# Optimization experiments

Measured on AMD Instinct MI355X. Metric: run time of the kernel, lower is better.

The kernel has to match this reference:

```python
import jax, jax.numpy as jnp
import numpy as np

N_NODES = 100000
N_EDGES = 1600000
IN_DIM, HID_DIM, OUT_DIM = 64, 64, 32


def setup_inputs() -> dict:
    key = jax.random.key(0)
    ks = jax.random.split(key, 8)
    s_in = 1.0 / np.sqrt(IN_DIM)
    s_hid = 1.0 / np.sqrt(HID_DIM)
    return {
        "x": jax.random.normal(ks[0], (N_NODES, IN_DIM), dtype=jnp.float32),
        "edge_index": jax.random.randint(ks[1], (2, N_EDGES), 0, N_NODES, dtype=jnp.int64),
        "W1l": jax.random.uniform(ks[2], (IN_DIM, HID_DIM), jnp.float32, -s_in, s_in),
        "b1l": jnp.zeros((HID_DIM,), jnp.float32),
        "W1r": jax.random.uniform(ks[3], (IN_DIM, HID_DIM), jnp.float32, -s_in, s_in),
        "W2l": jax.random.uniform(ks[4], (HID_DIM, OUT_DIM), jnp.float32, -s_hid, s_hid),
        "b2l": jnp.zeros((OUT_DIM,), jnp.float32),
        "W2r": jax.random.uniform(ks[5], (HID_DIM, OUT_DIM), jnp.float32, -s_hid, s_hid),
    }


def sage_conv(x, src, dst, W_l, b_l, W_r, n_nodes):
    # PyG SAGEConv (aggr='mean'): lin_l(mean of neighbor msgs) + lin_r(x)
    msg = x[src]                                                    # [E, d] gather
    agg = jax.ops.segment_sum(msg, dst, num_segments=n_nodes)      # [N, d] scatter-add
    deg = jax.ops.segment_sum(jnp.ones_like(dst, dtype=x.dtype), dst,
                              num_segments=n_nodes)
    agg = agg / jnp.maximum(deg, 1.0)[:, None]                     # mean (0 for isolated)
    return agg @ W_l + b_l + x @ W_r


def reference(x, edge_index, W1l, b1l, W1r, W2l, b2l, W2r):
    src, dst = edge_index[0], edge_index[1]
    n = x.shape[0]
    h = jax.nn.relu(sage_conv(x, src, dst, W1l, b1l, W1r, n))
    return sage_conv(h, src, dst, W2l, b2l, W2r, n)
```

## Files before the change

### kernel.cpp

```cpp
#include <hip/hip_runtime.h>

#define N_NODES 100000
#define N_EDGES 1600000
#define B2_SHIFT 9
#define BUCK_N (1 << B2_SHIFT)
#define NB2 ((N_NODES + BUCK_N - 1) >> B2_SHIFT)
#define BCAP 9216
#define PAIR_EPB 4096
#define PAIR_BLOCKS ((N_EDGES + PAIR_EPB - 1) / PAIR_EPB)
#define CAST_BLOCKS 6250
#define PREP_BLOCKS (PAIR_BLOCKS + 1 + CAST_BLOCKS)

typedef __attribute__((ext_vector_type(8))) short bf16x8;
typedef __attribute__((ext_vector_type(4))) float f32x4;

__device__ __forceinline__ unsigned pack2(float a, float b) {
    unsigned ua = __float_as_uint(a), ub = __float_as_uint(b);
    ua = (ua + 0x7FFFu + ((ua >> 16) & 1u)) >> 16;
    ub = (ub + 0x7FFFu + ((ub >> 16) & 1u)) >> 16;
    return ua | (ub << 16);
}
__device__ __forceinline__ float lo16(unsigned u) { return __uint_as_float(u << 16); }
__device__ __forceinline__ float hi16(unsigned u) { return __uint_as_float(u & 0xFFFF0000u); }

__global__ __launch_bounds__(256) void k_prep(
    const float* __restrict__ x, const int* __restrict__ ei,
    const float* __restrict__ W1l, const float* __restrict__ W1r,
    const float* __restrict__ W2l, const float* __restrict__ W2r,
    unsigned* __restrict__ xh, int* __restrict__ bcur,
    int* __restrict__ pairs, uint4* __restrict__ wf)
{
    __shared__ int lh[2][NB2];
    __shared__ int lb[2][NB2];

    if (blockIdx.x < PAIR_BLOCKS) {
        for (int i = threadIdx.x; i < NB2; i += 256) { lh[0][i] = 0; lh[1][i] = 0; }
        __syncthreads();
        int cp = (threadIdx.x >> 6) & 1;
        int base = blockIdx.x * PAIR_EPB;
        int myb[16], myr[16], myp[16];
#pragma unroll
        for (int t = 0; t < 16; t++) {
            int e = base + t * 256 + threadIdx.x;
            myb[t] = -1;
            if (e < N_EDGES) {
                int dst = ei[N_EDGES + e];
                int b = dst >> B2_SHIFT;
                myb[t] = b;
                myr[t] = atomicAdd(&lh[cp][b], 1);
                myp[t] = (ei[e] << B2_SHIFT) | (dst & (BUCK_N - 1));
            }
        }
        __syncthreads();
        for (int i = threadIdx.x; i < NB2; i += 256) {
            int c0 = lh[0][i], c1 = lh[1][i];
            int basei = (c0 + c1) ? atomicAdd(&bcur[i], c0 + c1) : 0;
            lb[0][i] = basei;
            lb[1][i] = basei + c0;
        }
        __syncthreads();
#pragma unroll
        for (int t = 0; t < 16; t++) {
            if (myb[t] >= 0) {
                int slot = lb[cp][myb[t]] + myr[t];
                if (slot < BCAP)
                    pairs[myb[t] * BCAP + slot] = myp[t];
            }
        }
    } else if (blockIdx.x == PAIR_BLOCKS) {
        for (int s = threadIdx.x; s < 1536; s += 256) {
            int f = s >> 6, l = s & 63;
            int m = l & 15, q = l >> 4;
            float w[8];
            if (f < 16) {
                int jt = f >> 2, ks = f & 3;
                int j = jt * 16 + m;
                int k0 = ks * 32 + q * 8;
#pragma unroll
                for (int i = 0; i < 8; i++) {
                    int kk = k0 + i;
                    w[i] = (kk < 64) ? W1l[kk * 64 + j] : W1r[(kk - 64) * 64 + j];
                }
            } else {
                int f2 = f - 16;
                int jt = f2 >> 1, ks = f2 & 1;
                int j = jt * 16 + m;
                int k0 = ks * 32 + q * 8;
#pragma unroll
                for (int i = 0; i < 8; i++) {
                    int kk = k0 + i;
                    w[i] = (j < 32) ? W2l[kk * 32 + j] : W2r[kk * 32 + (j - 32)];
                }
            }
            wf[s] = make_uint4(pack2(w[0], w[1]), pack2(w[2], w[3]),
                               pack2(w[4], w[5]), pack2(w[6], w[7]));
        }
    } else {
        int i = (blockIdx.x - PAIR_BLOCKS - 1) * 256 + threadIdx.x;
        if (i < N_NODES * 16) {
            float4 v = ((const float4*)x)[i];
            ((uint2*)xh)[i] = make_uint2(pack2(v.x, v.y), pack2(v.z, v.w));
        }
    }
}

__global__ __launch_bounds__(512) void k_sortb(const int* __restrict__ bcur,
                                               const int* __restrict__ pairs,
                                               int* __restrict__ sorted_src,
                                               int* __restrict__ rs,
                                               int* __restrict__ re)
{
    __shared__ int sp[BCAP];
    __shared__ int lcnt[BUCK_N];
    __shared__ int wtot[8];
    int b = blockIdx.x;
    int beg = b * BCAP;
    int cnt = bcur[b];
    if (cnt > BCAP) cnt = BCAP;
    for (int i = threadIdx.x; i < cnt; i += 512) sp[i] = pairs[beg + i];
    lcnt[threadIdx.x] = 0;
    __syncthreads();
    for (int i = threadIdx.x; i < cnt; i += 512)
        atomicAdd(&lcnt[sp[i] & (BUCK_N - 1)], 1);
    __syncthreads();
    int v = lcnt[threadIdx.x];
    int lane = threadIdx.x & 63, wid = threadIdx.x >> 6;
    int s = v;
#pragma unroll
    for (int off = 1; off < 64; off <<= 1) {
        int t = __shfl_up(s, off);
        if (lane >= off) s += t;
    }
    if (lane == 63) wtot[wid] = s;
    __syncthreads();
    int woff = 0;
#pragma unroll
    for (int k = 0; k < 8; k++) woff += (k < wid) ? wtot[k] : 0;
    int excl = woff + s - v;
    int n = (b << B2_SHIFT) + threadIdx.x;
    if (n < N_NODES) { rs[n] = beg + excl; re[n] = beg + excl + v; }
    __syncthreads();
    lcnt[threadIdx.x] = beg + excl;
    __syncthreads();
    for (int i = threadIdx.x; i < cnt; i += 512) {
        int p = sp[i];
        int idx = atomicAdd(&lcnt[p & (BUCK_N - 1)], 1);
        sorted_src[idx] = p >> B2_SHIFT;
    }
}

__global__ __launch_bounds__(256) void k_agg1(const int* __restrict__ rs,
                                              const int* __restrict__ re,
                                              const int* __restrict__ sorted_src,
                                              const unsigned* __restrict__ xh,
                                              unsigned* __restrict__ agg1h)
{
    int node = blockIdx.x * 8 + (threadIdx.x >> 5);
    if (node >= N_NODES) return;
    int d2 = threadIdx.x & 31;
    int beg = rs[node], end = re[node];
    float a0 = 0.f, a1 = 0.f, b0 = 0.f, b1 = 0.f;
    int idx = beg;
    for (; idx + 8 <= end; idx += 8) {
        int s0 = sorted_src[idx + 0], s1 = sorted_src[idx + 1];
        int s2 = sorted_src[idx + 2], s3 = sorted_src[idx + 3];
        int s4 = sorted_src[idx + 4], s5 = sorted_src[idx + 5];
        int s6 = sorted_src[idx + 6], s7 = sorted_src[idx + 7];
        unsigned p0 = xh[(size_t)s0 * 32 + d2];
        unsigned p1 = xh[(size_t)s1 * 32 + d2];
        unsigned p2 = xh[(size_t)s2 * 32 + d2];
        unsigned p3 = xh[(size_t)s3 * 32 + d2];
        unsigned p4 = xh[(size_t)s4 * 32 + d2];
        unsigned p5 = xh[(size_t)s5 * 32 + d2];
        unsigned p6 = xh[(size_t)s6 * 32 + d2];
        unsigned p7 = xh[(size_t)s7 * 32 + d2];
        a0 += lo16(p0) + lo16(p1);  a1 += hi16(p0) + hi16(p1);
        b0 += lo16(p2) + lo16(p3);  b1 += hi16(p2) + hi16(p3);
        a0 += lo16(p4) + lo16(p5);  a1 += hi16(p4) + hi16(p5);
        b0 += lo16(p6) + lo16(p7);  b1 += hi16(p6) + hi16(p7);
    }
    for (; idx + 2 <= end; idx += 2) {
        int s0 = sorted_src[idx], s1 = sorted_src[idx + 1];
        unsigned p0 = xh[(size_t)s0 * 32 + d2];
        unsigned p1 = xh[(size_t)s1 * 32 + d2];
        a0 += lo16(p0) + lo16(p1);  a1 += hi16(p0) + hi16(p1);
    }
    if (idx < end) {
        unsigned p = xh[(size_t)sorted_src[idx] * 32 + d2];
        a0 += lo16(p);  a1 += hi16(p);
    }
    agg1h[(size_t)node * 32 + d2] = pack2(a0 + b0, a1 + b1);
}

#define TPW 2
#define NTILE ((N_NODES + 15) / 16)
#define NODE_BLOCKS (((NTILE + TPW - 1) / TPW + 3) / 4)
__global__ __launch_bounds__(256) void k_node_mfma(
    const unsigned* __restrict__ xh, const unsigned* __restrict__ agg1h,
    const int* __restrict__ rs, const int* __restrict__ re,
    const float* __restrict__ b1l, const uint4* __restrict__ wf,
    unsigned* __restrict__ t2h, float* __restrict__ t3)
{
    __shared__ uint4 sWF[24 * 64];
    __shared__ float sH[4][16 * 68];
    __shared__ float sT[4][16 * 44];

    for (int s = threadIdx.x; s < 1536; s += 256)
        sWF[s] = wf[s];
    __syncthreads();

    int w = threadIdx.x >> 6, lane = threadIdx.x & 63;
    int m = lane & 15, q = lane >> 4;

    bf16x8 WF1[4][4], WF2[4][2];
#pragma unroll
    for (int jt = 0; jt < 4; jt++) {
#pragma unroll
        for (int ks = 0; ks < 4; ks++)
            WF1[jt][ks] = __builtin_bit_cast(bf16x8, sWF[(jt * 4 + ks) * 64 + lane]);
#pragma unroll
        for (int ks = 0; ks < 2; ks++)
            WF2[jt][ks] = __builtin_bit_cast(bf16x8, sWF[(16 + jt * 2 + ks) * 64 + lane]);
    }
    float bias[4];
#pragma unroll
    for (int jt = 0; jt < 4; jt++) bias[jt] = b1l[jt * 16 + m];

    float* myH = &sH[w][0];
    float* myT = &sT[w][0];
    int gw = blockIdx.x * 4 + w;

    for (int t = 0; t < TPW; t++) {
        int tile = gw * TPW + t;
        if (tile >= NTILE) break;
        int nb = tile * 16;

        int nc = nb + m; if (nc >= N_NODES) nc = N_NODES - 1;
        const uint4* arow = (const uint4*)(agg1h + (size_t)nc * 32);
        const uint4* xrow = (const uint4*)(xh + (size_t)nc * 32);
        bf16x8 AM[2], AX[2];
        AM[0] = __builtin_bit_cast(bf16x8, arow[q]);
        AM[1] = __builtin_bit_cast(bf16x8, arow[4 + q]);
        AX[0] = __builtin_bit_cast(bf16x8, xrow[q]);
        AX[1] = __builtin_bit_cast(bf16x8, xrow[4 + q]);

        float invr[4];
#pragma unroll
        for (int r = 0; r < 4; r++) {
            int nn = nb + q * 4 + r;
            int nc2 = (nn < N_NODES) ? nn : 0;
            invr[r] = 1.0f / fmaxf((float)(re[nc2] - rs[nc2]), 1.0f);
        }

#pragma unroll
        for (int jt = 0; jt < 4; jt++) {
            f32x4 aM = {0.f, 0.f, 0.f, 0.f}, aX = {0.f, 0.f, 0.f, 0.f};
            aM = __builtin_amdgcn_mfma_f32_16x16x32_bf16(AM[0], WF1[jt][0], aM, 0, 0, 0);
            aM = __builtin_amdgcn_mfma_f32_16x16x32_bf16(AM[1], WF1[jt][1], aM, 0, 0, 0);
            aX = __builtin_amdgcn_mfma_f32_16x16x32_bf16(AX[0], WF1[jt][2], aX, 0, 0, 0);
            aX = __builtin_amdgcn_mfma_f32_16x16x32_bf16(AX[1], WF1[jt][3], aX, 0, 0, 0);
#pragma unroll
            for (int r = 0; r < 4; r++) {
                float hv = fmaxf(aM[r] * invr[r] + aX[r] + bias[jt], 0.0f);
                myH[(q * 4 + r) * 68 + jt * 16 + m] = hv;
            }
        }

        bf16x8 A2[2];
#pragma unroll
        for (int ks = 0; ks < 2; ks++) {
            const float* p = &myH[m * 68 + ks * 32 + q * 8];
            float4 v0 = *(const float4*)p;
            float4 v1 = *(const float4*)(p + 4);
            uint4 u = make_uint4(pack2(v0.x, v0.y), pack2(v0.z, v0.w),
                                 pack2(v1.x, v1.y), pack2(v1.z, v1.w));
            A2[ks] = __builtin_bit_cast(bf16x8, u);
        }

#pragma unroll
        for (int jt = 0; jt < 4; jt++) {
            f32x4 acc = {0.f, 0.f, 0.f, 0.f};
            acc = __builtin_amdgcn_mfma_f32_16x16x32_bf16(A2[0], WF2[jt][0], acc, 0, 0, 0);
            acc = __builtin_amdgcn_mfma_f32_16x16x32_bf16(A2[1], WF2[jt][1], acc, 0, 0, 0);
            if (jt < 2) {
#pragma unroll
                for (int r = 0; r < 4; r++)
                    myT[(q * 4 + r) * 44 + jt * 16 + m] = acc[r];
            } else {
#pragma unroll
                for (int r = 0; r < 4; r++) {
                    int nn = nb + q * 4 + r;
                    if (nn < N_NODES)
                        t3[(size_t)nn * 32 + (jt - 2) * 16 + m] = acc[r];
                }
            }
        }

        int ni = lane >> 2, u4g = lane & 3;
        const float* tp = &myT[ni * 44 + u4g * 8];
        float4 a = *(const float4*)tp;
        float4 b = *(const float4*)(tp + 4);
        if (nb + ni < N_NODES) {
            uint4 o = make_uint4(pack2(a.x, a.y), pack2(a.z, a.w),
                                 pack2(b.x, b.y), pack2(b.z, b.w));
            *(uint4*)(t2h + (size_t)(nb + ni) * 16 + u4g * 4) = o;
        }
    }
}

__global__ __launch_bounds__(256) void k_agg2out(
    const int* __restrict__ rs, const int* __restrict__ re,
    const int* __restrict__ sorted_src,
    const unsigned* __restrict__ t2h, const float* __restrict__ t3,
    const float* __restrict__ b2l, float* __restrict__ out)
{
    int node = blockIdx.x * 16 + (threadIdx.x >> 4);
    if (node >= N_NODES) return;
    int d2 = threadIdx.x & 15;
    int beg = rs[node], end = re[node];
    float a0 = 0.f, a1 = 0.f, b0 = 0.f, b1 = 0.f;
    int idx = beg;
    for (; idx + 8 <= end; idx += 8) {
        int s0 = sorted_src[idx + 0], s1 = sorted_src[idx + 1];
        int s2 = sorted_src[idx + 2], s3 = sorted_src[idx + 3];
        int s4 = sorted_src[idx + 4], s5 = sorted_src[idx + 5];
        int s6 = sorted_src[idx + 6], s7 = sorted_src[idx + 7];
        unsigned p0 = t2h[(size_t)s0 * 16 + d2];
        unsigned p1 = t2h[(size_t)s1 * 16 + d2];
        unsigned p2 = t2h[(size_t)s2 * 16 + d2];
        unsigned p3 = t2h[(size_t)s3 * 16 + d2];
        unsigned p4 = t2h[(size_t)s4 * 16 + d2];
        unsigned p5 = t2h[(size_t)s5 * 16 + d2];
        unsigned p6 = t2h[(size_t)s6 * 16 + d2];
        unsigned p7 = t2h[(size_t)s7 * 16 + d2];
        a0 += lo16(p0) + lo16(p1);  a1 += hi16(p0) + hi16(p1);
        b0 += lo16(p2) + lo16(p3);  b1 += hi16(p2) + hi16(p3);
        a0 += lo16(p4) + lo16(p5);  a1 += hi16(p4) + hi16(p5);
        b0 += lo16(p6) + lo16(p7);  b1 += hi16(p6) + hi16(p7);
    }
    for (; idx + 2 <= end; idx += 2) {
        int s0 = sorted_src[idx], s1 = sorted_src[idx + 1];
        unsigned p0 = t2h[(size_t)s0 * 16 + d2];
        unsigned p1 = t2h[(size_t)s1 * 16 + d2];
        a0 += lo16(p0) + lo16(p1);  a1 += hi16(p0) + hi16(p1);
    }
    if (idx < end) {
        unsigned p = t2h[(size_t)sorted_src[idx] * 16 + d2];
        a0 += lo16(p);  a1 += hi16(p);
    }
    float inv = 1.0f / fmaxf((float)(end - beg), 1.0f);
    float2 tv = ((const float2*)(t3 + (size_t)node * 32))[d2];
    float2 bv = ((const float2*)b2l)[d2];
    ((float2*)(out + (size_t)node * 32))[d2] =
        make_float2((a0 + b0) * inv + tv.x + bv.x,
                    (a1 + b1) * inv + tv.y + bv.y);
}

extern "C" void kernel_launch(void* const* d_in, const int* in_sizes, int n_in,
                              void* d_out, int out_size, void* d_ws, size_t ws_size,
                              hipStream_t stream) {
    const float* x   = (const float*)d_in[0];
    const int*   ei  = (const int*)d_in[1];
    const float* W1l = (const float*)d_in[2];
    const float* b1l = (const float*)d_in[3];
    const float* W1r = (const float*)d_in[4];
    const float* W2l = (const float*)d_in[5];
    const float* b2l = (const float*)d_in[6];
    const float* W2r = (const float*)d_in[7];
    float* out = (float*)d_out;

    const size_t N = N_NODES;
    int* wsi = (int*)d_ws;
    int*      pairs      = wsi;
    int*      sorted_src = wsi + 1806336;
    int*      bcur       = wsi + 3612672;
    int*      rs         = wsi + 3612928;
    int*      re         = wsi + 3712928;
    unsigned* xh         = (unsigned*)(wsi + 3812928);
    unsigned* t2h        = xh + 32 * N;
    unsigned* agg1h      = t2h + 16 * N;
    float*    t3         = (float*)(agg1h + 32 * N);
    uint4*    wf         = (uint4*)(t3 + 32 * N);

    hipMemsetAsync(bcur, 0, NB2 * sizeof(int), stream);
    k_prep <<<PREP_BLOCKS, 256, 0, stream>>>(x, ei, W1l, W1r, W2l, W2r,
                                             xh, bcur, pairs, wf);
    k_sortb<<<NB2, 512, 0, stream>>>(bcur, pairs, sorted_src, rs, re);

    k_agg1     <<<(int)((N + 7) / 8), 256, 0, stream>>>(rs, re, sorted_src, xh, agg1h);
    k_node_mfma<<<NODE_BLOCKS, 256, 0, stream>>>(xh, agg1h, rs, re,
                                                 b1l, wf, t2h, t3);
    k_agg2out  <<<(int)((N + 15) / 16), 256, 0, stream>>>(rs, re, sorted_src,
                                                 t2h, t3, b2l, out);
}
```

Baseline: 200.2 us.

## Fuse layer-1 neighbor aggregation into the MFMA node kernel

Measured after the change: 259.0 us. 29.4% more time.

```diff
diff --git a/kernel.cpp b/kernel.cpp
--- a/kernel.cpp
+++ b/kernel.cpp
@@ -149,56 +149,15 @@
     }
 }
 
-__global__ __launch_bounds__(256) void k_agg1(const int* __restrict__ rs,
-                                              const int* __restrict__ re,
-                                              const int* __restrict__ sorted_src,
-                                              const unsigned* __restrict__ xh,
-                                              unsigned* __restrict__ agg1h)
-{
-    int node = blockIdx.x * 8 + (threadIdx.x >> 5);
-    if (node >= N_NODES) return;
-    int d2 = threadIdx.x & 31;
-    int beg = rs[node], end = re[node];
-    float a0 = 0.f, a1 = 0.f, b0 = 0.f, b1 = 0.f;
-    int idx = beg;
-    for (; idx + 8 <= end; idx += 8) {
-        int s0 = sorted_src[idx + 0], s1 = sorted_src[idx + 1];
-        int s2 = sorted_src[idx + 2], s3 = sorted_src[idx + 3];
-        int s4 = sorted_src[idx + 4], s5 = sorted_src[idx + 5];
-        int s6 = sorted_src[idx + 6], s7 = sorted_src[idx + 7];
-        unsigned p0 = xh[(size_t)s0 * 32 + d2];
-        unsigned p1 = xh[(size_t)s1 * 32 + d2];
-        unsigned p2 = xh[(size_t)s2 * 32 + d2];
-        unsigned p3 = xh[(size_t)s3 * 32 + d2];
-        unsigned p4 = xh[(size_t)s4 * 32 + d2];
-        unsigned p5 = xh[(size_t)s5 * 32 + d2];
-        unsigned p6 = xh[(size_t)s6 * 32 + d2];
-        unsigned p7 = xh[(size_t)s7 * 32 + d2];
-        a0 += lo16(p0) + lo16(p1);  a1 += hi16(p0) + hi16(p1);
-        b0 += lo16(p2) + lo16(p3);  b1 += hi16(p2) + hi16(p3);
-        a0 += lo16(p4) + lo16(p5);  a1 += hi16(p4) + hi16(p5);
-        b0 += lo16(p6) + lo16(p7);  b1 += hi16(p6) + hi16(p7);
-    }
-    for (; idx + 2 <= end; idx += 2) {
-        int s0 = sorted_src[idx], s1 = sorted_src[idx + 1];
-        unsigned p0 = xh[(size_t)s0 * 32 + d2];
-        unsigned p1 = xh[(size_t)s1 * 32 + d2];
-        a0 += lo16(p0) + lo16(p1);  a1 += hi16(p0) + hi16(p1);
-    }
-    if (idx < end) {
-        unsigned p = xh[(size_t)sorted_src[idx] * 32 + d2];
-        a0 += lo16(p);  a1 += hi16(p);
-    }
-    agg1h[(size_t)node * 32 + d2] = pack2(a0 + b0, a1 + b1);
-}
-
 #define TPW 2
 #define NTILE ((N_NODES + 15) / 16)
 #define NODE_BLOCKS (((NTILE + TPW - 1) / TPW + 3) / 4)
 __global__ __launch_bounds__(256) void k_node_mfma(
-    const unsigned* __restrict__ xh, const unsigned* __restrict__ agg1h,
+    const unsigned* __restrict__ xh,
     const int* __restrict__ rs, const int* __restrict__ re,
-    const float* __restrict__ b1l, const uint4* __restrict__ wf,
+    const int* __restrict__ sorted_src,
+    const float* __restrict__ b1l, const float* __restrict__ b2l,
+    const uint4* __restrict__ wf,
     unsigned* __restrict__ t2h, float* __restrict__ t3)
 {
     __shared__ uint4 sWF[24 * 64];
@@ -211,20 +170,12 @@
 
     int w = threadIdx.x >> 6, lane = threadIdx.x & 63;
     int m = lane & 15, q = lane >> 4;
-
-    bf16x8 WF1[4][4], WF2[4][2];
-#pragma unroll
-    for (int jt = 0; jt < 4; jt++) {
-#pragma unroll
-        for (int ks = 0; ks < 4; ks++)
-            WF1[jt][ks] = __builtin_bit_cast(bf16x8, sWF[(jt * 4 + ks) * 64 + lane]);
-#pragma unroll
-        for (int ks = 0; ks < 2; ks++)
-            WF2[jt][ks] = __builtin_bit_cast(bf16x8, sWF[(16 + jt * 2 + ks) * 64 + lane]);
-    }
+    int half = lane >> 5, d2g = lane & 31;
+
     float bias[4];
 #pragma unroll
     for (int jt = 0; jt < 4; jt++) bias[jt] = b1l[jt * 16 + m];
+    float bias2[2] = { b2l[m], b2l[16 + m] };
 
     float* myH = &sH[w][0];
     float* myT = &sT[w][0];
@@ -235,12 +186,57 @@
         if (tile >= NTILE) break;
         int nb = tile * 16;
 
+        for (int p = 0; p < 8; p++) {
+            int node = nb + 2 * p + half;
+            float a0 = 0.f, a1 = 0.f, c0 = 0.f, c1 = 0.f;
+            if (node < N_NODES) {
+                int beg = rs[node], end = re[node];
+                int idx = beg;
+                for (; idx + 8 <= end; idx += 8) {
+                    int s0 = sorted_src[idx + 0], s1 = sorted_src[idx + 1];
+                    int s2 = sorted_src[idx + 2], s3 = sorted_src[idx + 3];
+                    int s4 = sorted_src[idx + 4], s5 = sorted_src[idx + 5];
+                    int s6 = sorted_src[idx + 6], s7 = sorted_src[idx + 7];
+                    unsigned p0 = xh[(size_t)s0 * 32 + d2g];
+                    unsigned p1 = xh[(size_t)s1 * 32 + d2g];
+                    unsigned p2 = xh[(size_t)s2 * 32 + d2g];
+                    unsigned p3 = xh[(size_t)s3 * 32 + d2g];
+                    unsigned p4 = xh[(size_t)s4 * 32 + d2g];
+                    unsigned p5 = xh[(size_t)s5 * 32 + d2g];
+                    unsigned p6 = xh[(size_t)s6 * 32 + d2g];
+                    unsigned p7 = xh[(size_t)s7 * 32 + d2g];
+                    a0 += lo16(p0) + lo16(p1);  a1 += hi16(p0) + hi16(p1);
+                    c0 += lo16(p2) + lo16(p3);  c1 += hi16(p2) + hi16(p3);
+                    a0 += lo16(p4) + lo16(p5);  a1 += hi16(p4) + hi16(p5);
+                    c0 += lo16(p6) + lo16(p7);  c1 += hi16(p6) + hi16(p7);
+                }
+                for (; idx + 2 <= end; idx += 2) {
+                    int s0 = sorted_src[idx], s1 = sorted_src[idx + 1];
+                    unsigned p0 = xh[(size_t)s0 * 32 + d2g];
+                    unsigned p1 = xh[(size_t)s1 * 32 + d2g];
+                    a0 += lo16(p0) + lo16(p1);  a1 += hi16(p0) + hi16(p1);
+                }
+                if (idx < end) {
+                    unsigned p0 = xh[(size_t)sorted_src[idx] * 32 + d2g];
+                    a0 += lo16(p0);  a1 += hi16(p0);
+                }
+            }
+            *(float2*)&myH[(2 * p + half) * 68 + 2 * d2g] =
+                make_float2(a0 + c0, a1 + c1);
+        }
+
         int nc = nb + m; if (nc >= N_NODES) nc = N_NODES - 1;
-        const uint4* arow = (const uint4*)(agg1h + (size_t)nc * 32);
+        bf16x8 AM[2], AX[2];
+#pragma unroll
+        for (int ks = 0; ks < 2; ks++) {
+            const float* pH = &myH[m * 68 + ks * 32 + q * 8];
+            float4 v0 = *(const float4*)pH;
+            float4 v1 = *(const float4*)(pH + 4);
+            uint4 u = make_uint4(pack2(v0.x, v0.y), pack2(v0.z, v0.w),
+                                 pack2(v1.x, v1.y), pack2(v1.z, v1.w));
+            AM[ks] = __builtin_bit_cast(bf16x8, u);
+        }
         const uint4* xrow = (const uint4*)(xh + (size_t)nc * 32);
-        bf16x8 AM[2], AX[2];
-        AM[0] = __builtin_bit_cast(bf16x8, arow[q]);
-        AM[1] = __builtin_bit_cast(bf16x8, arow[4 + q]);
         AX[0] = __builtin_bit_cast(bf16x8, xrow[q]);
         AX[1] = __builtin_bit_cast(bf16x8, xrow[4 + q]);
 
@@ -255,10 +251,14 @@
 #pragma unroll
         for (int jt = 0; jt < 4; jt++) {
             f32x4 aM = {0.f, 0.f, 0.f, 0.f}, aX = {0.f, 0.f, 0.f, 0.f};
-            aM = __builtin_amdgcn_mfma_f32_16x16x32_bf16(AM[0], WF1[jt][0], aM, 0, 0, 0);
-            aM = __builtin_amdgcn_mfma_f32_16x16x32_bf16(AM[1], WF1[jt][1], aM, 0, 0, 0);
-            aX = __builtin_amdgcn_mfma_f32_16x16x32_bf16(AX[0], WF1[jt][2], aX, 0, 0, 0);
-            aX = __builtin_amdgcn_mfma_f32_16x16x32_bf16(AX[1], WF1[jt][3], aX, 0, 0, 0);
+            aM = __builtin_amdgcn_mfma_f32_16x16x32_bf16(
+                AM[0], __builtin_bit_cast(bf16x8, sWF[(jt * 4 + 0) * 64 + lane]), aM, 0, 0, 0);
+            aM = __builtin_amdgcn_mfma_f32_16x16x32_bf16(
+                AM[1], __builtin_bit_cast(bf16x8, sWF[(jt * 4 + 1) * 64 + lane]), aM, 0, 0, 0);
+            aX = __builtin_amdgcn_mfma_f32_16x16x32_bf16(
+                AX[0], __builtin_bit_cast(bf16x8, sWF[(jt * 4 + 2) * 64 + lane]), aX, 0, 0, 0);
+            aX = __builtin_amdgcn_mfma_f32_16x16x32_bf16(
+                AX[1], __builtin_bit_cast(bf16x8, sWF[(jt * 4 + 3) * 64 + lane]), aX, 0, 0, 0);
 #pragma unroll
             for (int r = 0; r < 4; r++) {
                 float hv = fmaxf(aM[r] * invr[r] + aX[r] + bias[jt], 0.0f);
@@ -280,8 +280,10 @@
 #pragma unroll
         for (int jt = 0; jt < 4; jt++) {
             f32x4 acc = {0.f, 0.f, 0.f, 0.f};
-            acc = __builtin_amdgcn_mfma_f32_16x16x32_bf16(A2[0], WF2[jt][0], acc, 0, 0, 0);
-            acc = __builtin_amdgcn_mfma_f32_16x16x32_bf16(A2[1], WF2[jt][1], acc, 0, 0, 0);
+            acc = __builtin_amdgcn_mfma_f32_16x16x32_bf16(
+                A2[0], __builtin_bit_cast(bf16x8, sWF[(16 + jt * 2 + 0) * 64 + lane]), acc, 0, 0, 0);
+            acc = __builtin_amdgcn_mfma_f32_16x16x32_bf16(
+                A2[1], __builtin_bit_cast(bf16x8, sWF[(16 + jt * 2 + 1) * 64 + lane]), acc, 0, 0, 0);
             if (jt < 2) {
 #pragma unroll
                 for (int r = 0; r < 4; r++)
@@ -291,7 +293,7 @@
                 for (int r = 0; r < 4; r++) {
                     int nn = nb + q * 4 + r;
                     if (nn < N_NODES)
-                        t3[(size_t)nn * 32 + (jt - 2) * 16 + m] = acc[r];
+                        t3[(size_t)nn * 32 + (jt - 2) * 16 + m] = acc[r] + bias2[jt - 2];
                 }
             }
         }
@@ -312,7 +314,7 @@
     const int* __restrict__ rs, const int* __restrict__ re,
     const int* __restrict__ sorted_src,
     const unsigned* __restrict__ t2h, const float* __restrict__ t3,
-    const float* __restrict__ b2l, float* __restrict__ out)
+    float* __restrict__ out)
 {
     int node = blockIdx.x * 16 + (threadIdx.x >> 4);
     if (node >= N_NODES) return;
@@ -350,10 +352,9 @@
     }
     float inv = 1.0f / fmaxf((float)(end - beg), 1.0f);
     float2 tv = ((const float2*)(t3 + (size_t)node * 32))[d2];
-    float2 bv = ((const float2*)b2l)[d2];
     ((float2*)(out + (size_t)node * 32))[d2] =
-        make_float2((a0 + b0) * inv + tv.x + bv.x,
-                    (a1 + b1) * inv + tv.y + bv.y);
+        make_float2((a0 + b0) * inv + tv.x,
+                    (a1 + b1) * inv + tv.y);
 }
 
 extern "C" void kernel_launch(void* const* d_in, const int* in_sizes, int n_in,
@@ -378,8 +379,7 @@
     int*      re         = wsi + 3712928;
     unsigned* xh         = (unsigned*)(wsi + 3812928);
     unsigned* t2h        = xh + 32 * N;
-    unsigned* agg1h      = t2h + 16 * N;
-    float*    t3         = (float*)(agg1h + 32 * N);
+    float*    t3         = (float*)(t2h + 16 * N);
     uint4*    wf         = (uint4*)(t3 + 32 * N);
 
     hipMemsetAsync(bcur, 0, NB2 * sizeof(int), stream);
@@ -387,9 +387,8 @@
                                              xh, bcur, pairs, wf);
     k_sortb<<<NB2, 512, 0, stream>>>(bcur, pairs, sorted_src, rs, re);
 
-    k_agg1     <<<(int)((N + 7) / 8), 256, 0, stream>>>(rs, re, sorted_src, xh, agg1h);
-    k_node_mfma<<<NODE_BLOCKS, 256, 0, stream>>>(xh, agg1h, rs, re,
-                                                 b1l, wf, t2h, t3);
+    k_node_mfma<<<NODE_BLOCKS, 256, 0, stream>>>(xh, rs, re, sorted_src,
+                                                 b1l, b2l, wf, t2h, t3);
     k_agg2out  <<<(int)((N + 15) / 16), 256, 0, stream>>>(rs, re, sorted_src,
-                                                 t2h, t3, b2l, out);
-}
+                                                 t2h, t3, out);
+}
```
